# Optimization experiments

Hardware: AMD Instinct MI355X
Metric: run time of the kernel (lower is better)

## Reference

```python
import jax, jax.numpy as jnp
import numpy as np

D, N = 512, 128

def setup_inputs() -> dict:
    key = jax.random.key(0)
    k1, k2 = jax.random.split(key)
    A = jax.random.normal(k1, (D, D), dtype=jnp.float32)
    Q, _ = jnp.linalg.qr(A)                      # orthonormal orbitals (reortho_orbitals QR)
    P = Q[:, :N].astype(jnp.float32)             # D x N Slater orbitals
    positions = jnp.sort(jax.random.choice(k2, D, shape=(N,), replace=False)).astype(jnp.int32)
    return {"P": P, "positions": positions}


def _lu_pivots(A):
    """Diagonal of U from unpivoted Gaussian elimination.
    Leading principal minors of A are cumulative products of these pivots."""
    Dn = A.shape[-1]
    idx = jnp.arange(Dn)
    def step(M, j):
        pivot = M[j, j]
        col = jnp.where(idx > j, M[:, j] / pivot, 0.0)   # elimination multipliers
        M = M - col[:, None] * M[j][None, :]             # rank-1 update (memory bound)
        return M, pivot
    _, piv = jax.lax.scan(step, A, idx)
    return piv


def _cond_probs(P, positions):
    dtype = P.dtype
    G = jnp.eye(D, dtype=dtype) - P @ P.T                 # D x D
    onehots = jax.nn.one_hot(positions, D, dtype=dtype)   # [N, D]
    occ_prefix = jnp.cumsum(onehots, axis=0) - onehots    # occ of sites chosen before step k
    # A_k = G - diag(occ_prefix[k]): denominator/base matrix of step k
    A = G[None, :, :] - occ_prefix[:, :, None] * jnp.eye(D, dtype=dtype)[None]
    piv = jax.vmap(_lu_pivots)(A)                         # [N, D] pivots u_jj
    k = jnp.arange(N)
    xmin = jnp.where(k == 0, 0, positions[jnp.maximum(k - 1, 0)] + 1)  # [N]
    xmax = D - N + k + 1
    i = jnp.arange(D)[None, :]
    # probs[k,i] = -(det Gnum)/(det Gdenom) = (1 - u_ii) * prod_{j=xmin..i-1} u_jj
    q = jnp.where(i >= xmin[:, None], piv, jnp.ones((), dtype))
    c = jnp.concatenate([jnp.ones((N, 1), dtype), jnp.cumprod(q, axis=1)[:, :-1]], axis=1)
    probs = c * (1.0 - piv)
    valid = (i >= xmin[:, None]) & (i < xmax[:, None])
    probs = jnp.where(valid, probs, 0.0)
    probs = jnp.where(jnp.abs(probs) > 1e-15, probs, 0.0)  # torch.where(|p|>1e-15, p, 0)
    return probs


def reference(P, positions):
    probs = _cond_probs(P, positions)                     # [N, D] conditional distributions
    picked = jnp.take_along_axis(probs, positions[:, None], axis=1)[:, 0]
    log_prob_sample = jnp.sum(jnp.log(picked))            # log of prob_sample (product underflows)
    return probs, log_prob_sample
```

## Files before the change

### kernel.cpp

```cpp
#include <hip/hip_runtime.h>
#include <math.h>

#define DD 512
#define NN 128
#define XBASE 385

#define OFF_M      0
#define OFF_LP     262144
#define OFF_UP     278528
#define OFF_CPIV   294912
#define OFF_SHAD   295424
#define OFF_SSNAP  295552
#define OFF_FPIV   297600
#define OFF_LOG    363136
#define OFF_MI     363264
#define OFF_POSMAP 364032
#define OFF_MISC   364544
#define OFF_FORK   364608

template<bool RECALL>
__device__ __forceinline__ float w0_block_lu(float (&a)[32], float sh,
    unsigned long long shmask, int elim, int recl,
    float* __restrict__ pvsL, float (*dblkL)[33],
    float* __restrict__ recp, int gbase, int gmin, int lane)
{
    bool mine = (shmask >> lane) & 1ull;
#pragma unroll
    for (int j = 0; j < 32; ++j) {
        if (j > recl) break;
        float d  = __shfl(a[j], j);
        float sj = __shfl(sh, j);
        if (lane == 0) {
            int g = gbase + j;
            if (RECALL || g > gmin) recp[g] = d;
        }
        if (j >= elim) break;
        float pv = ((shmask >> j) & 1ull) ? sj : d;
        if (lane == 0) pvsL[j] = pv;
        bool below = lane > j;
        if (below) a[j] = a[j] / pv;
        float m = a[j];
#pragma unroll
        for (int c = j + 1; c < 32; ++c) {
            float bj = __shfl(a[c], j);
            if (below) {
                a[c] = fmaf(-m, bj, a[c]);
                if (mine && lane == c) sh = fmaf(-m, bj, sh);
            }
        }
    }
#pragma unroll
    for (int c = 0; c < 32; ++c) dblkL[lane][c] = a[c];
    return sh;
}

__global__ void k_build(const float* __restrict__ P, float* __restrict__ ws) {
    __shared__ float Pr[32][129];
    __shared__ float Pc[32][129];
    int r0 = blockIdx.x * 32, c0 = blockIdx.y * 32, tid = threadIdx.x;
    for (int idx = tid; idx < 32 * 128; idx += 256) {
        int r = idx >> 7, t = idx & 127;
        Pr[r][t] = P[(r0 + r) * NN + t];
        Pc[r][t] = P[(c0 + r) * NN + t];
    }
    __syncthreads();
    int cl = tid & 31, rl0 = tid >> 5;
    for (int e = 0; e < 4; ++e) {
        int rl = rl0 + e * 8;
        float acc = 0.0f;
#pragma unroll 8
        for (int t = 0; t < 128; ++t) acc = fmaf(Pr[rl][t], Pc[cl][t], acc);
        int gr = r0 + rl, gc = c0 + cl;
        ws[OFF_M + gr * DD + gc] = ((gr == gc) ? 1.0f : 0.0f) - acc;
    }
}

__global__ void k_meta(const int* __restrict__ pos, float* __restrict__ ws) {
    int* mi   = (int*)ws + OFF_MI;
    int* pm   = (int*)ws + OFF_POSMAP;
    int* misc = (int*)ws + OFF_MISC;
    __shared__ int sS[128];
    int k = threadIdx.x;
    int p = pos[k];
    mi[k] = p;
    mi[128 + k] = (k == 0) ? 0 : (pos[k - 1] + 1);
    int x = XBASE + k;
    mi[256 + k] = x;
    int j0 = (p >> 5) << 5;
    mi[384 + k] = j0;
    int s = x - j0;
    mi[512 + k] = s;
    sS[k] = s * s;
    float g = ws[OFF_M + p * DD + p];
    ws[OFF_SHAD + k]  = g - 1.0f;
    ws[OFF_SSNAP + k] = g - 1.0f;
    for (int i = k; i < 512; i += 128) pm[i] = -1;
    __syncthreads();
    pm[p] = k;
    if (k == 0) {
        int acc = 0;
        for (int i = 0; i < 128; ++i) { mi[640 + i] = acc; acc += sS[i]; }
        misc[0] = pos[127];
    }
}

__global__ void k_snap0(float* __restrict__ ws) {
    const int* mi = (const int*)ws + OFF_MI;
    int r0 = blockIdx.x * 32, c0 = blockIdx.y * 32, tid = threadIdx.x;
    int cl = tid & 31, rl0 = tid >> 5;
    for (int k = 0; k < 128; ++k) {
        if (mi[384 + k] != 0) continue;
        int x = mi[256 + k];
        if (r0 >= x || c0 >= x) continue;
        int s = mi[512 + k];
        float* buf = ws + OFF_FORK + mi[640 + k];
        for (int e = 0; e < 4; ++e) {
            int gr = r0 + rl0 + e * 8, gc = c0 + cl;
            if (gr < x && gc < x) buf[gr * s + gc] = ws[OFF_M + gr * DD + gc];
        }
    }
}

__global__ void __launch_bounds__(1024) k_panel(float* __restrict__ ws, int t) {
    const int* misc = (const int*)ws + OFF_MISC;
    int j0 = t * 32;
    if (j0 > misc[0]) return;
    const int* pm = (const int*)ws + OFF_POSMAP;
    __shared__ float dblk[32][33];
    __shared__ float pvs[32];
    __shared__ float shadL[128];
    __shared__ int   chfL[32];
    int tid = threadIdx.x;
    int jn = j0 + 32, w = DD - jn;
    if (tid < 128) { float sv = ws[OFF_SHAD + tid]; shadL[tid] = sv; ws[OFF_SSNAP + t * 128 + tid] = sv; }
    if (tid < 32) chfL[tid] = pm[j0 + tid];
    __syncthreads();
    if (tid < 32) {
        float a[32];
#pragma unroll
        for (int c = 0; c < 32; ++c) a[c] = ws[OFF_M + (size_t)(j0 + tid) * DD + j0 + c];
        int cf = chfL[tid];
        float sh = (cf >= 0) ? shadL[cf] : 0.0f;
        unsigned long long bm = __ballot(cf >= 0);
        sh = w0_block_lu<true>(a, sh, bm, 32, 31, pvs, dblk, ws + OFF_CPIV, j0, -1, tid);
        if (cf >= 0) ws[OFF_SHAD + cf] = sh;
    }
    __syncthreads();
    for (int task = tid; task < 2 * w; task += 1024) {
        if (task < w) {
            int r = jn + task;
            const float* src = ws + OFF_M + (size_t)r * DD + j0;
            float a[32];
#pragma unroll
            for (int c = 0; c < 32; ++c) a[c] = src[c];
#pragma unroll
            for (int j = 0; j < 32; ++j) {
                float tv = a[j];
                for (int c = 0; c < j; ++c) tv = fmaf(-a[c], dblk[c][j], tv);
                a[j] = tv / pvs[j];
            }
            float* dst = ws + OFF_LP + (size_t)r * 32;
#pragma unroll
            for (int c = 0; c < 32; ++c) dst[c] = a[c];
        } else {
            int col = jn + (task - w);
            float v[32];
#pragma unroll
            for (int j = 0; j < 32; ++j) v[j] = ws[OFF_M + (size_t)(j0 + j) * DD + col];
#pragma unroll
            for (int j = 1; j < 32; ++j) {
                float tv = v[j];
                for (int c = 0; c < j; ++c) tv = fmaf(-dblk[j][c], v[c], tv);
                v[j] = tv;
            }
#pragma unroll
            for (int j = 0; j < 32; ++j) ws[OFF_UP + j * DD + col] = v[j];
        }
    }
}

__global__ void k_trail(float* __restrict__ ws, int t) {
    const int* misc = (const int*)ws + OFF_MISC;
    int j0 = t * 32, jn = j0 + 32;
    if (jn > misc[0]) return;
    const int* mi = (const int*)ws + OFF_MI;
    const int* pm = (const int*)ws + OFF_POSMAP;
    int r0 = blockIdx.x * 32, c0 = blockIdx.y * 32, tid = threadIdx.x;
    if (r0 < jn || c0 < jn) return;
    __shared__ float Mt[32][33], Lt[32][33], Ut[32][33];
    int cl = tid & 31, rl0 = tid >> 5;
    for (int e = 0; e < 4; ++e) {
        int rl = rl0 + e * 8;
        Mt[rl][cl] = ws[OFF_M + (r0 + rl) * DD + c0 + cl];
        Lt[rl][cl] = ws[OFF_LP + (r0 + rl) * 32 + cl];
        Ut[rl][cl] = ws[OFF_UP + rl * DD + c0 + cl];
    }
    __syncthreads();
    for (int e = 0; e < 4; ++e) {
        int rl = rl0 + e * 8;
        float acc = Mt[rl][cl];
#pragma unroll
        for (int jj = 0; jj < 32; ++jj) acc = fmaf(-Lt[rl][jj], Ut[jj][cl], acc);
        Mt[rl][cl] = acc;
        int gr = r0 + rl, gc = c0 + cl;
        if (gr == gc) {
            int kk = pm[gr];
            if (kk >= 0) {
                float sv = ws[OFF_SHAD + kk];
#pragma unroll
                for (int jj = 0; jj < 32; ++jj) sv = fmaf(-Lt[rl][jj], Ut[jj][cl], sv);
                ws[OFF_SHAD + kk] = sv;
            }
        }
        ws[OFF_M + gr * DD + gc] = acc;
    }
    __syncthreads();
    for (int k = 0; k < 128; ++k) {
        if (mi[384 + k] != jn) continue;
        int x = mi[256 + k];
        if (r0 >= x || c0 >= x) continue;
        int s = mi[512 + k];
        float* buf = ws + OFF_FORK + mi[640 + k];
        for (int e = 0; e < 4; ++e) {
            int gr = r0 + rl0 + e * 8, gc = c0 + cl;
            if (gr < x && gc < x) buf[(gr - jn) * s + (gc - jn)] = Mt[rl0 + e * 8][cl];
        }
    }
}

__global__ void __launch_bounds__(1024) k_fork(float* __restrict__ ws) {
    const int* mi = (const int*)ws + OFF_MI;
    const int* pm = (const int*)ws + OFF_POSMAP;
    int k = blockIdx.x;
    int p = mi[k], x = mi[256 + k], j0 = mi[384 + k], s = mi[512 + k];
    if (p >= x - 1) return;
    float* buf = ws + OFF_FORK + mi[640 + k];
    float* fpv = ws + OFF_FPIV + k * DD;
    int tstage = j0 >> 5;
    __shared__ float dblk[32][33];
    __shared__ float pvs[32];
    __shared__ float fpan[388][33];
    __shared__ float fstrip[32][388];
    int tid = threadIdx.x;
    int xl = s - 1;
    for (int pf0 = 0;; pf0 += 32) {
        int rem = xl - pf0;
        if (tid < 32) {
            float a[32];
#pragma unroll
            for (int c = 0; c < 32; ++c) {
                int rr = pf0 + tid, cc = pf0 + c;
                a[c] = (rr <= xl && cc <= xl) ? buf[(size_t)rr * s + cc] : 0.0f;
            }
            float sh = 0.0f;
            unsigned long long bm = 0ull;
            if (pf0 == 0) {
                int g = j0 + tid;
                int kk = pm[g];
                bool ch = (kk >= 0 && g < p);
                if (ch) sh = ws[OFF_SSNAP + tstage * 128 + kk];
                bm = __ballot(ch);
            }
            int elim = rem < 32 ? rem : 32;
            int recl = rem < 31 ? rem : 31;
            w0_block_lu<false>(a, sh, bm, elim, recl, pvs, dblk, fpv, j0 + pf0, p, tid);
        }
        if (rem < 32) break;
        __syncthreads();
        int tw = s - pf0 - 32;
        if (tid < tw) {
            int r = pf0 + 32 + tid;
            const float* src = buf + (size_t)r * s + pf0;
            float a[32];
#pragma unroll
            for (int c = 0; c < 32; ++c) a[c] = src[c];
#pragma unroll
            for (int j = 0; j < 32; ++j) {
                float tv = a[j];
                for (int c = 0; c < j; ++c) tv = fmaf(-a[c], dblk[c][j], tv);
                a[j] = tv / pvs[j];
            }
#pragma unroll
            for (int c = 0; c < 32; ++c) fpan[tid][c] = a[c];
        } else if (tid >= 512 && tid < 512 + tw) {
            int u = tid - 512;
            int col = pf0 + 32 + u;
            float v[32];
#pragma unroll
            for (int j = 0; j < 32; ++j) v[j] = buf[(size_t)(pf0 + j) * s + col];
#pragma unroll
            for (int j = 1; j < 32; ++j) {
                float tv = v[j];
                for (int c = 0; c < j; ++c) tv = fmaf(-dblk[j][c], v[c], tv);
                v[j] = tv;
            }
#pragma unroll
            for (int j = 0; j < 32; ++j) fstrip[j][u] = v[j];
        }
        __syncthreads();
        {
            int ntr = (tw + 3) >> 2;
            int nt2 = ntr * ntr;
            for (int tile = tid; tile < nt2; tile += 1024) {
                int ti = tile / ntr;
                int tr = ti << 2, tc = (tile - ti * ntr) << 2;
                int rb = pf0 + 32 + tr, cb = pf0 + 32 + tc;
                float acc[4][4];
                if (tr + 4 <= tw && tc + 4 <= tw) {
#pragma unroll
                    for (int i = 0; i < 4; ++i)
#pragma unroll
                        for (int j = 0; j < 4; ++j) acc[i][j] = buf[(size_t)(rb + i) * s + cb + j];
#pragma unroll 8
                    for (int jj = 0; jj < 32; ++jj) {
                        float a0 = fpan[tr + 0][jj], a1 = fpan[tr + 1][jj];
                        float a2 = fpan[tr + 2][jj], a3 = fpan[tr + 3][jj];
                        float b0 = fstrip[jj][tc + 0], b1 = fstrip[jj][tc + 1];
                        float b2 = fstrip[jj][tc + 2], b3 = fstrip[jj][tc + 3];
                        acc[0][0] = fmaf(-a0, b0, acc[0][0]); acc[0][1] = fmaf(-a0, b1, acc[0][1]);
                        acc[0][2] = fmaf(-a0, b2, acc[0][2]); acc[0][3] = fmaf(-a0, b3, acc[0][3]);
                        acc[1][0] = fmaf(-a1, b0, acc[1][0]); acc[1][1] = fmaf(-a1, b1, acc[1][1]);
                        acc[1][2] = fmaf(-a1, b2, acc[1][2]); acc[1][3] = fmaf(-a1, b3, acc[1][3]);
                        acc[2][0] = fmaf(-a2, b0, acc[2][0]); acc[2][1] = fmaf(-a2, b1, acc[2][1]);
                        acc[2][2] = fmaf(-a2, b2, acc[2][2]); acc[2][3] = fmaf(-a2, b3, acc[2][3]);
                        acc[3][0] = fmaf(-a3, b0, acc[3][0]); acc[3][1] = fmaf(-a3, b1, acc[3][1]);
                        acc[3][2] = fmaf(-a3, b2, acc[3][2]); acc[3][3] = fmaf(-a3, b3, acc[3][3]);
                    }
#pragma unroll
                    for (int i = 0; i < 4; ++i)
#pragma unroll
                        for (int j = 0; j < 4; ++j) buf[(size_t)(rb + i) * s + cb + j] = acc[i][j];
                } else {
#pragma unroll
                    for (int i = 0; i < 4; ++i)
#pragma unroll
                        for (int j = 0; j < 4; ++j)
                            acc[i][j] = (tr + i < tw && tc + j < tw) ? buf[(size_t)(rb + i) * s + cb + j] : 0.0f;
                    for (int jj = 0; jj < 32; ++jj) {
                        float a[4], b[4];
#pragma unroll
                        for (int i = 0; i < 4; ++i) {
                            int rr = tr + i; a[i] = fpan[rr < tw ? rr : (tw - 1)][jj];
                        }
#pragma unroll
                        for (int j = 0; j < 4; ++j) {
                            int ccc = tc + j; b[j] = fstrip[jj][ccc < tw ? ccc : (tw - 1)];
                        }
#pragma unroll
                        for (int i = 0; i < 4; ++i)
#pragma unroll
                            for (int j = 0; j < 4; ++j) acc[i][j] = fmaf(-a[i], b[j], acc[i][j]);
                    }
#pragma unroll
                    for (int i = 0; i < 4; ++i)
#pragma unroll
                        for (int j = 0; j < 4; ++j)
                            if (tr + i < tw && tc + j < tw) buf[(size_t)(rb + i) * s + cb + j] = acc[i][j];
                }
            }
        }
        __syncthreads();
    }
}

__global__ void k_epilogue(float* __restrict__ ws, float* __restrict__ out) {
    const int* mi = (const int*)ws + OFF_MI;
    int k = blockIdx.x, tid = threadIdx.x;
    __shared__ float row[512];
    __shared__ float pivs[512];
    int c = mi[128 + k], p = mi[k], x = mi[256 + k];
    for (int i = tid; i < 512; i += 256) {
        row[i] = 0.0f;
        pivs[i] = (i <= p) ? ws[OFF_CPIV + i] : ws[OFF_FPIV + k * DD + i];
    }
    __syncthreads();
    if (tid == 0) {
        float cp = 1.0f;
        for (int i = c; i < x; ++i) {
            float pv = pivs[i];
            float pr = cp * (1.0f - pv);
            row[i] = (fabsf(pr) > 1e-15f) ? pr : 0.0f;
            cp = cp * pv;
        }
        ws[OFF_LOG + k] = logf(row[p]);
    }
    __syncthreads();
    for (int i = tid; i < 512; i += 256) out[k * DD + i] = row[i];
}

__global__ void k_logsum(float* __restrict__ ws, float* __restrict__ out) {
    __shared__ float lv[128];
    int tid = threadIdx.x;
    if (tid < 64) { lv[tid] = ws[OFF_LOG + tid]; lv[tid + 64] = ws[OFF_LOG + tid + 64]; }
    __syncthreads();
    if (tid == 0) {
        double sacc = 0.0;
        for (int i = 0; i < 128; ++i) sacc += (double)lv[i];
        out[65536] = (float)sacc;
    }
}

extern "C" void kernel_launch(void* const* d_in, const int* in_sizes, int n_in,
                              void* d_out, int out_size, void* d_ws, size_t ws_size,
                              hipStream_t stream) {
    const float* P   = (const float*)d_in[0];
    const int*   pos = (const int*)d_in[1];
    float* ws  = (float*)d_ws;
    float* out = (float*)d_out;

    k_build<<<dim3(16, 16), 256, 0, stream>>>(P, ws);
    k_meta<<<1, 128, 0, stream>>>(pos, ws);
    k_snap0<<<dim3(16, 16), 256, 0, stream>>>(ws);
    for (int t = 0; t < 16; ++t) {
        k_panel<<<1, 1024, 0, stream>>>(ws, t);
        if (t < 15) k_trail<<<dim3(16, 16), 256, 0, stream>>>(ws, t);
    }
    k_fork<<<128, 1024, 0, stream>>>(ws);
    k_epilogue<<<128, 256, 0, stream>>>(ws, out);
    k_logsum<<<1, 64, 0, stream>>>(ws, out);
}
```

Before: 2.318 ms.

## Vectorize panel solves, register-tile trailing update, widen fork GEMM tiles

Rewrites the panel triangular solves as right-looking updates that read the diagonal block, and a new transposed copy of it, with float4 shared-memory loads. The trailing-update kernel now keeps a 1x4 output strip per thread in registers instead of staging the M tile in shared memory, which drops a shared buffer and a barrier. The fork kernel's in-block GEMM moves from 4x4 to 8x8 register tiles and reads a transposed panel with float4. These changes target shared-memory traffic and instruction overhead, at the cost of more registers per thread (64 accumulators in the fork kernel) and possible lower occupancy.

```diff
diff --git a/kernel.cpp b/kernel.cpp
--- a/kernel.cpp
+++ b/kernel.cpp
@@ -21,7 +21,7 @@
 template<bool RECALL>
 __device__ __forceinline__ float w0_block_lu(float (&a)[32], float sh,
     unsigned long long shmask, int elim, int recl,
-    float* __restrict__ pvsL, float (*dblkL)[33],
+    float* __restrict__ pvsL, float (*dblkL)[36], float (*dblkTL)[36],
     float* __restrict__ recp, int gbase, int gmin, int lane)
 {
     bool mine = (shmask >> lane) & 1ull;
@@ -50,8 +50,42 @@
         }
     }
 #pragma unroll
-    for (int c = 0; c < 32; ++c) dblkL[lane][c] = a[c];
+    for (int c = 0; c < 32; ++c) { dblkL[lane][c] = a[c]; dblkTL[c][lane] = a[c]; }
     return sh;
+}
+
+__device__ __forceinline__ void solve_L21_row(float (&a)[32], const float (*dblk)[36],
+                                              const float* __restrict__ pvs) {
+#pragma unroll
+    for (int c = 0; c < 32; ++c) {
+        a[c] = a[c] / pvs[c];
+        float m = a[c];
+        int j = c + 1;
+#pragma unroll
+        for (; (j & 3) && j < 32; ++j) a[j] = fmaf(-m, dblk[c][j], a[j]);
+#pragma unroll
+        for (; j + 3 < 32; j += 4) {
+            const float4 u = *(const float4*)&dblk[c][j];
+            a[j+0] = fmaf(-m, u.x, a[j+0]); a[j+1] = fmaf(-m, u.y, a[j+1]);
+            a[j+2] = fmaf(-m, u.z, a[j+2]); a[j+3] = fmaf(-m, u.w, a[j+3]);
+        }
+    }
+}
+
+__device__ __forceinline__ void solve_U12_col(float (&v)[32], const float (*dblkT)[36]) {
+#pragma unroll
+    for (int c = 0; c < 31; ++c) {
+        float vc = v[c];
+        int j = c + 1;
+#pragma unroll
+        for (; (j & 3) && j < 32; ++j) v[j] = fmaf(-dblkT[c][j], vc, v[j]);
+#pragma unroll
+        for (; j + 3 < 32; j += 4) {
+            const float4 u = *(const float4*)&dblkT[c][j];
+            v[j+0] = fmaf(-u.x, vc, v[j+0]); v[j+1] = fmaf(-u.y, vc, v[j+1]);
+            v[j+2] = fmaf(-u.z, vc, v[j+2]); v[j+3] = fmaf(-u.w, vc, v[j+3]);
+        }
+    }
 }
 
 __global__ void k_build(const float* __restrict__ P, float* __restrict__ ws) {
@@ -126,7 +160,7 @@
     int j0 = t * 32;
     if (j0 > misc[0]) return;
     const int* pm = (const int*)ws + OFF_POSMAP;
-    __shared__ float dblk[32][33];
+    __shared__ float dblk[32][36], dblkT[32][36];
     __shared__ float pvs[32];
     __shared__ float shadL[128];
     __shared__ int   chfL[32];
@@ -142,7 +176,7 @@
         int cf = chfL[tid];
         float sh = (cf >= 0) ? shadL[cf] : 0.0f;
         unsigned long long bm = __ballot(cf >= 0);
-        sh = w0_block_lu<true>(a, sh, bm, 32, 31, pvs, dblk, ws + OFF_CPIV, j0, -1, tid);
+        sh = w0_block_lu<true>(a, sh, bm, 32, 31, pvs, dblk, dblkT, ws + OFF_CPIV, j0, -1, tid);
         if (cf >= 0) ws[OFF_SHAD + cf] = sh;
     }
     __syncthreads();
@@ -153,12 +187,7 @@
             float a[32];
 #pragma unroll
             for (int c = 0; c < 32; ++c) a[c] = src[c];
-#pragma unroll
-            for (int j = 0; j < 32; ++j) {
-                float tv = a[j];
-                for (int c = 0; c < j; ++c) tv = fmaf(-a[c], dblk[c][j], tv);
-                a[j] = tv / pvs[j];
-            }
+            solve_L21_row(a, dblk, pvs);
             float* dst = ws + OFF_LP + (size_t)r * 32;
 #pragma unroll
             for (int c = 0; c < 32; ++c) dst[c] = a[c];
@@ -167,12 +196,7 @@
             float v[32];
 #pragma unroll
             for (int j = 0; j < 32; ++j) v[j] = ws[OFF_M + (size_t)(j0 + j) * DD + col];
-#pragma unroll
-            for (int j = 1; j < 32; ++j) {
-                float tv = v[j];
-                for (int c = 0; c < j; ++c) tv = fmaf(-dblk[j][c], v[c], tv);
-                v[j] = tv;
-            }
+            solve_U12_col(v, dblkT);
 #pragma unroll
             for (int j = 0; j < 32; ++j) ws[OFF_UP + j * DD + col] = v[j];
         }
@@ -187,43 +211,47 @@
     const int* pm = (const int*)ws + OFF_POSMAP;
     int r0 = blockIdx.x * 32, c0 = blockIdx.y * 32, tid = threadIdx.x;
     if (r0 < jn || c0 < jn) return;
-    __shared__ float Mt[32][33], Lt[32][33], Ut[32][33];
+    __shared__ float Lt[32][36], Ut[32][36];
     int cl = tid & 31, rl0 = tid >> 5;
     for (int e = 0; e < 4; ++e) {
         int rl = rl0 + e * 8;
-        Mt[rl][cl] = ws[OFF_M + (r0 + rl) * DD + c0 + cl];
         Lt[rl][cl] = ws[OFF_LP + (r0 + rl) * 32 + cl];
         Ut[rl][cl] = ws[OFF_UP + rl * DD + c0 + cl];
     }
     __syncthreads();
-    for (int e = 0; e < 4; ++e) {
-        int rl = rl0 + e * 8;
-        float acc = Mt[rl][cl];
-#pragma unroll
-        for (int jj = 0; jj < 32; ++jj) acc = fmaf(-Lt[rl][jj], Ut[jj][cl], acc);
-        Mt[rl][cl] = acc;
-        int gr = r0 + rl, gc = c0 + cl;
-        if (gr == gc) {
-            int kk = pm[gr];
-            if (kk >= 0) {
-                float sv = ws[OFF_SHAD + kk];
-#pragma unroll
-                for (int jj = 0; jj < 32; ++jj) sv = fmaf(-Lt[rl][jj], Ut[jj][cl], sv);
-                ws[OFF_SHAD + kk] = sv;
-            }
-        }
-        ws[OFF_M + gr * DD + gc] = acc;
-    }
-    __syncthreads();
+    int r = tid >> 3, c4 = (tid & 7) << 2;
+    int gr = r0 + r;
+    float acc[4];
+#pragma unroll
+    for (int j = 0; j < 4; ++j) acc[j] = ws[OFF_M + (size_t)gr * DD + c0 + c4 + j];
+#pragma unroll 8
+    for (int jj = 0; jj < 32; ++jj) {
+        float lv = Lt[r][jj];
+        const float4 uv = *(const float4*)&Ut[jj][c4];
+        acc[0] = fmaf(-lv, uv.x, acc[0]); acc[1] = fmaf(-lv, uv.y, acc[1]);
+        acc[2] = fmaf(-lv, uv.z, acc[2]); acc[3] = fmaf(-lv, uv.w, acc[3]);
+    }
+    if (r0 == c0 && r >= c4 && r < c4 + 4) {
+        int kk = pm[gr];
+        if (kk >= 0) {
+            float sv = ws[OFF_SHAD + kk];
+#pragma unroll 8
+            for (int jj = 0; jj < 32; ++jj) sv = fmaf(-Lt[r][jj], Ut[jj][r], sv);
+            ws[OFF_SHAD + kk] = sv;
+        }
+    }
+#pragma unroll
+    for (int j = 0; j < 4; ++j) ws[OFF_M + (size_t)gr * DD + c0 + c4 + j] = acc[j];
     for (int k = 0; k < 128; ++k) {
         if (mi[384 + k] != jn) continue;
         int x = mi[256 + k];
-        if (r0 >= x || c0 >= x) continue;
+        if (r0 >= x || c0 >= x || gr >= x) continue;
         int s = mi[512 + k];
         float* buf = ws + OFF_FORK + mi[640 + k];
-        for (int e = 0; e < 4; ++e) {
-            int gr = r0 + rl0 + e * 8, gc = c0 + cl;
-            if (gr < x && gc < x) buf[(gr - jn) * s + (gc - jn)] = Mt[rl0 + e * 8][cl];
+#pragma unroll
+        for (int j = 0; j < 4; ++j) {
+            int gc = c0 + c4 + j;
+            if (gc < x) buf[(size_t)(gr - jn) * s + (gc - jn)] = acc[j];
         }
     }
 }
@@ -237,10 +265,10 @@
     float* buf = ws + OFF_FORK + mi[640 + k];
     float* fpv = ws + OFF_FPIV + k * DD;
     int tstage = j0 >> 5;
-    __shared__ float dblk[32][33];
+    __shared__ float dblk[32][36], dblkT[32][36];
     __shared__ float pvs[32];
-    __shared__ float fpan[388][33];
-    __shared__ float fstrip[32][388];
+    __shared__ float fpanT[32][360];
+    __shared__ float fstrip[32][360];
     int tid = threadIdx.x;
     int xl = s - 1;
     for (int pf0 = 0;; pf0 += 32) {
@@ -263,7 +291,7 @@
             }
             int elim = rem < 32 ? rem : 32;
             int recl = rem < 31 ? rem : 31;
-            w0_block_lu<false>(a, sh, bm, elim, recl, pvs, dblk, fpv, j0 + pf0, p, tid);
+            w0_block_lu<false>(a, sh, bm, elim, recl, pvs, dblk, dblkT, fpv, j0 + pf0, p, tid);
         }
         if (rem < 32) break;
         __syncthreads();
@@ -274,88 +302,77 @@
             float a[32];
 #pragma unroll
             for (int c = 0; c < 32; ++c) a[c] = src[c];
-#pragma unroll
-            for (int j = 0; j < 32; ++j) {
-                float tv = a[j];
-                for (int c = 0; c < j; ++c) tv = fmaf(-a[c], dblk[c][j], tv);
-                a[j] = tv / pvs[j];
-            }
-#pragma unroll
-            for (int c = 0; c < 32; ++c) fpan[tid][c] = a[c];
+            solve_L21_row(a, dblk, pvs);
+#pragma unroll
+            for (int c = 0; c < 32; ++c) fpanT[c][tid] = a[c];
         } else if (tid >= 512 && tid < 512 + tw) {
             int u = tid - 512;
             int col = pf0 + 32 + u;
             float v[32];
 #pragma unroll
             for (int j = 0; j < 32; ++j) v[j] = buf[(size_t)(pf0 + j) * s + col];
-#pragma unroll
-            for (int j = 1; j < 32; ++j) {
-                float tv = v[j];
-                for (int c = 0; c < j; ++c) tv = fmaf(-dblk[j][c], v[c], tv);
-                v[j] = tv;
-            }
+            solve_U12_col(v, dblkT);
 #pragma unroll
             for (int j = 0; j < 32; ++j) fstrip[j][u] = v[j];
         }
         __syncthreads();
         {
-            int ntr = (tw + 3) >> 2;
+            int ntr = (tw + 7) >> 3;
             int nt2 = ntr * ntr;
             for (int tile = tid; tile < nt2; tile += 1024) {
                 int ti = tile / ntr;
-                int tr = ti << 2, tc = (tile - ti * ntr) << 2;
+                int tr = ti << 3, tc = (tile - ti * ntr) << 3;
                 int rb = pf0 + 32 + tr, cb = pf0 + 32 + tc;
-                float acc[4][4];
-                if (tr + 4 <= tw && tc + 4 <= tw) {
-#pragma unroll
-                    for (int i = 0; i < 4; ++i)
-#pragma unroll
-                        for (int j = 0; j < 4; ++j) acc[i][j] = buf[(size_t)(rb + i) * s + cb + j];
-#pragma unroll 8
+                if (tr + 8 <= tw && tc + 8 <= tw) {
+                    float acc[8][8];
+#pragma unroll
+                    for (int i = 0; i < 8; ++i)
+#pragma unroll
+                        for (int j = 0; j < 8; ++j) acc[i][j] = buf[(size_t)(rb + i) * s + cb + j];
+#pragma unroll 2
                     for (int jj = 0; jj < 32; ++jj) {
-                        float a0 = fpan[tr + 0][jj], a1 = fpan[tr + 1][jj];
-                        float a2 = fpan[tr + 2][jj], a3 = fpan[tr + 3][jj];
-                        float b0 = fstrip[jj][tc + 0], b1 = fstrip[jj][tc + 1];
-                        float b2 = fstrip[jj][tc + 2], b3 = fstrip[jj][tc + 3];
-                        acc[0][0] = fmaf(-a0, b0, acc[0][0]); acc[0][1] = fmaf(-a0, b1, acc[0][1]);
-                        acc[0][2] = fmaf(-a0, b2, acc[0][2]); acc[0][3] = fmaf(-a0, b3, acc[0][3]);
-                        acc[1][0] = fmaf(-a1, b0, acc[1][0]); acc[1][1] = fmaf(-a1, b1, acc[1][1]);
-                        acc[1][2] = fmaf(-a1, b2, acc[1][2]); acc[1][3] = fmaf(-a1, b3, acc[1][3]);
-                        acc[2][0] = fmaf(-a2, b0, acc[2][0]); acc[2][1] = fmaf(-a2, b1, acc[2][1]);
-                        acc[2][2] = fmaf(-a2, b2, acc[2][2]); acc[2][3] = fmaf(-a2, b3, acc[2][3]);
-                        acc[3][0] = fmaf(-a3, b0, acc[3][0]); acc[3][1] = fmaf(-a3, b1, acc[3][1]);
-                        acc[3][2] = fmaf(-a3, b2, acc[3][2]); acc[3][3] = fmaf(-a3, b3, acc[3][3]);
+                        const float4 a0 = *(const float4*)&fpanT[jj][tr];
+                        const float4 a1 = *(const float4*)&fpanT[jj][tr + 4];
+                        const float4 b0 = *(const float4*)&fstrip[jj][tc];
+                        const float4 b1 = *(const float4*)&fstrip[jj][tc + 4];
+                        float av[8] = {a0.x, a0.y, a0.z, a0.w, a1.x, a1.y, a1.z, a1.w};
+                        float bv[8] = {b0.x, b0.y, b0.z, b0.w, b1.x, b1.y, b1.z, b1.w};
+#pragma unroll
+                        for (int i = 0; i < 8; ++i)
+#pragma unroll
+                            for (int j = 0; j < 8; ++j)
+                                acc[i][j] = fmaf(-av[i], bv[j], acc[i][j]);
                     }
 #pragma unroll
-                    for (int i = 0; i < 4; ++i)
-#pragma unroll
-                        for (int j = 0; j < 4; ++j) buf[(size_t)(rb + i) * s + cb + j] = acc[i][j];
+                    for (int i = 0; i < 8; ++i)
+#pragma unroll
+                        for (int j = 0; j < 8; ++j) buf[(size_t)(rb + i) * s + cb + j] = acc[i][j];
                 } else {
-#pragma unroll
-                    for (int i = 0; i < 4; ++i)
-#pragma unroll
-                        for (int j = 0; j < 4; ++j)
-                            acc[i][j] = (tr + i < tw && tc + j < tw) ? buf[(size_t)(rb + i) * s + cb + j] : 0.0f;
+                    int nr = tw - tr; nr = nr > 8 ? 8 : nr;
+                    int nc = tw - tc; nc = nc > 8 ? 8 : nc;
+                    float acc[8][8];
+#pragma unroll
+                    for (int i = 0; i < 8; ++i)
+#pragma unroll
+                        for (int j = 0; j < 8; ++j)
+                            acc[i][j] = (i < nr && j < nc) ? buf[(size_t)(rb + i) * s + cb + j] : 0.0f;
                     for (int jj = 0; jj < 32; ++jj) {
-                        float a[4], b[4];
-#pragma unroll
-                        for (int i = 0; i < 4; ++i) {
-                            int rr = tr + i; a[i] = fpan[rr < tw ? rr : (tw - 1)][jj];
-                        }
-#pragma unroll
-                        for (int j = 0; j < 4; ++j) {
-                            int ccc = tc + j; b[j] = fstrip[jj][ccc < tw ? ccc : (tw - 1)];
-                        }
-#pragma unroll
-                        for (int i = 0; i < 4; ++i)
-#pragma unroll
-                            for (int j = 0; j < 4; ++j) acc[i][j] = fmaf(-a[i], b[j], acc[i][j]);
+                        float av[8], bv[8];
+#pragma unroll
+                        for (int i = 0; i < 8; ++i) av[i] = (i < nr) ? fpanT[jj][tr + i] : 0.0f;
+#pragma unroll
+                        for (int j = 0; j < 8; ++j) bv[j] = (j < nc) ? fstrip[jj][tc + j] : 0.0f;
+#pragma unroll
+                        for (int i = 0; i < 8; ++i)
+#pragma unroll
+                            for (int j = 0; j < 8; ++j)
+                                acc[i][j] = fmaf(-av[i], bv[j], acc[i][j]);
                     }
 #pragma unroll
-                    for (int i = 0; i < 4; ++i)
-#pragma unroll
-                        for (int j = 0; j < 4; ++j)
-                            if (tr + i < tw && tc + j < tw) buf[(size_t)(rb + i) * s + cb + j] = acc[i][j];
+                    for (int i = 0; i < 8; ++i)
+#pragma unroll
+                        for (int j = 0; j < 8; ++j)
+                            if (i < nr && j < nc) buf[(size_t)(rb + i) * s + cb + j] = acc[i][j];
                 }
             }
         }
```

Measured after the change: 2.136 ms. 1.09x faster.
